# Kernel optimization log

Hardware: AMD Instinct MI355X
Metric: run time of the kernel (lower is better)

Reference implementation:

```python
import jax, jax.numpy as jnp
import numpy as np

T, B, H, K = 512, 64, 512, 16  # seq_len, batch, hidden_size, num_tags


def setup_inputs() -> dict:
    key = jax.random.key(0)
    ks = jax.random.split(key, 8)
    hidden = jax.random.normal(ks[0], (T, B, H), dtype=jnp.float32)
    W1 = jax.random.normal(ks[1], (H, H), dtype=jnp.float32) / np.float32(np.sqrt(H))
    b1 = jnp.zeros((H,), jnp.float32)
    W2 = jax.random.normal(ks[2], (H, K), dtype=jnp.float32) / np.float32(np.sqrt(H))
    b2 = jnp.zeros((K,), jnp.float32)
    transition = jax.random.normal(ks[3], (K, K), dtype=jnp.float32)
    lens = jax.random.randint(ks[4], (B,), T // 2, T + 1)  # valid lengths in [T/2, T]
    tags = jax.random.randint(ks[5], (T, B), 0, K)
    return dict(hidden=hidden, W1=W1, b1=b1, W2=W2, b2=b2,
                transition=transition, lens=lens, tags=tags)


def reference(hidden, W1, b1, W2, b2, transition, lens, tags):
    # Emission MLP (dropout is identity in eval): Linear -> ReLU -> Linear
    h = jax.nn.relu(hidden @ W1 + b1)          # [T, B, H]
    em = h @ W2 + b2                           # [T, B, K]

    # ---- forward (partition) score: linear-chain logsumexp DP ----
    def step(alpha, e_t):
        # alpha: [B, K] over prev tags; transition[curr, prev]
        a = jax.nn.logsumexp(alpha[:, None, :] + transition[None, :, :], axis=-1) + e_t
        return a, a

    alpha0 = em[0]
    _, alphas = jax.lax.scan(step, alpha0, em[1:])
    alphas = jnp.concatenate([alpha0[None], alphas], axis=0)            # [T, B, K]
    last = jnp.take_along_axis(alphas, (lens - 1)[None, :, None], axis=0)[0]  # [B, K]
    fwd_score = jax.nn.logsumexp(last, axis=-1)                          # [B]

    # ---- gold path score ----
    em_path = jnp.take_along_axis(em, tags[:, :, None], axis=-1)[..., 0]  # [T, B]
    trans_path = transition[tags[1:], tags[:-1]]                          # [T-1, B]
    steps = em_path.at[1:].add(trans_path)
    cum = jnp.cumsum(steps, axis=0)                                       # [T, B]
    gold = jnp.take_along_axis(cum, (lens - 1)[None, :], axis=0)[0]       # [B]

    return (fwd_score - gold).sum()
```

## Files before the change

### kernel.cpp

```cpp
#include <hip/hip_runtime.h>
#include <hip/hip_bf16.h>

#define TT 512
#define BB 64
#define HH 512
#define KK 16

#define NCH 16
#define CST (TT / NCH)

typedef __attribute__((ext_vector_type(8))) short bf16x8;
typedef __attribute__((ext_vector_type(4))) short bf16x4;
typedef __attribute__((ext_vector_type(4))) float f32x4;

#define MFMA_K16(A, B, C) __builtin_amdgcn_mfma_f32_16x16x16bf16_1k(A, B, C, 0, 0, 0)

__device__ __forceinline__ unsigned short f2bf(float f) {
    union { __hip_bfloat16 h; unsigned short u; } cvt;
    cvt.h = __float2bfloat16(f);
    return cvt.u;
}

__device__ __forceinline__ short rne_bf(float x) {
    unsigned u = __float_as_uint(x);
    u += 0x7fffu + ((u >> 16) & 1u);
    return (short)(u >> 16);
}

__device__ __forceinline__ float bf2f(short s) {
    return __uint_as_float(((unsigned)(unsigned short)s) << 16);
}

__global__ void prep_kernel(const float* __restrict__ W1, const float* __restrict__ W2,
                            unsigned short* __restrict__ W1t, unsigned short* __restrict__ W2t,
                            float* __restrict__ out) {
    const int bi = blockIdx.x, tx = threadIdx.x;
    if (bi < 64) {
        __shared__ float Ls[64][65];
        const int ti = bi & 7, tj = bi >> 3;
        const int r0 = ti * 64, c0 = tj * 64;
        const int r = tx >> 4, c4 = (tx & 15) * 4;
#pragma unroll
        for (int i = 0; i < 4; ++i) {
            float4 v = *(const float4*)(W1 + (size_t)(r0 + r + 16 * i) * HH + c0 + c4);
            Ls[c4 + 0][r + 16 * i] = v.x;
            Ls[c4 + 1][r + 16 * i] = v.y;
            Ls[c4 + 2][r + 16 * i] = v.z;
            Ls[c4 + 3][r + 16 * i] = v.w;
        }
        __syncthreads();
        const int rn = tx >> 4, k4 = (tx & 15) * 4;
#pragma unroll
        for (int i = 0; i < 4; ++i) {
            const int n = rn + 16 * i;
            ushort4 o;
            o.x = f2bf(Ls[n][k4 + 0]);
            o.y = f2bf(Ls[n][k4 + 1]);
            o.z = f2bf(Ls[n][k4 + 2]);
            o.w = f2bf(Ls[n][k4 + 3]);
            *(ushort4*)(W1t + (size_t)(c0 + n) * HH + r0 + k4) = o;
        }
    } else {
        if (tx == 0) out[0] = 0.0f;
        for (int idx = tx; idx < 16 * HH; idx += 256) {
            const int n = idx >> 9, k = idx & 511;
            W2t[idx] = f2bf(W2[k * KK + n]);
        }
    }
}

__global__ __launch_bounds__(256, 2)
void em_kernel(const float* __restrict__ hidden, const unsigned short* __restrict__ W1t,
               const float* __restrict__ b1, const unsigned short* __restrict__ W2t,
               const float* __restrict__ b2, float* __restrict__ em) {
    __shared__ __align__(16) unsigned char stage[74752];
    unsigned short* const As = (unsigned short*)stage;
    unsigned short* const Bs = (unsigned short*)(stage + 9216);

    const int tx = threadIdx.x;
    const int w = tx >> 6, lane = tx & 63;
    const int q = lane >> 4, nl = lane & 15;
    const int wm = w >> 1, wn = w & 1;
    const int row0 = blockIdx.x * 64;

    f32x4 acc[2][16];
#pragma unroll
    for (int mt = 0; mt < 2; ++mt)
#pragma unroll
        for (int nt = 0; nt < 16; ++nt) acc[mt][nt] = (f32x4){0.f, 0.f, 0.f, 0.f};

    for (int kt = 0; kt < 8; ++kt) {
        const int k0 = kt * 64;
        __syncthreads();
        {
            const int r = tx >> 2, c16 = (tx & 3) * 16;
            const float* src = hidden + (size_t)(row0 + r) * HH + k0 + c16;
            float4 v0 = *(const float4*)(src);
            float4 v1 = *(const float4*)(src + 4);
            float4 v2 = *(const float4*)(src + 8);
            float4 v3 = *(const float4*)(src + 12);
            bf16x8 o0, o1;
            o0[0] = (short)f2bf(v0.x); o0[1] = (short)f2bf(v0.y);
            o0[2] = (short)f2bf(v0.z); o0[3] = (short)f2bf(v0.w);
            o0[4] = (short)f2bf(v1.x); o0[5] = (short)f2bf(v1.y);
            o0[6] = (short)f2bf(v1.z); o0[7] = (short)f2bf(v1.w);
            o1[0] = (short)f2bf(v2.x); o1[1] = (short)f2bf(v2.y);
            o1[2] = (short)f2bf(v2.z); o1[3] = (short)f2bf(v2.w);
            o1[4] = (short)f2bf(v3.x); o1[5] = (short)f2bf(v3.y);
            o1[6] = (short)f2bf(v3.z); o1[7] = (short)f2bf(v3.w);
            *(bf16x8*)(As + r * 72 + c16) = o0;
            *(bf16x8*)(As + r * 72 + c16 + 8) = o1;
        }
#pragma unroll
        for (int it = 0; it < 16; ++it) {
            const int c = it * 256 + tx;
            const int n = c >> 3, slot = c & 7;
            const int kc = slot ^ (n & 7);
            __builtin_amdgcn_global_load_lds(
                (const __attribute__((address_space(1))) void*)(W1t + (size_t)n * HH + k0 + kc * 8),
                (__attribute__((address_space(3))) void*)(Bs + c * 8),
                16, 0, 0);
        }
        __syncthreads();
        bf16x8 af[2][2];
#pragma unroll
        for (int mt = 0; mt < 2; ++mt)
#pragma unroll
            for (int kk = 0; kk < 2; ++kk)
                af[mt][kk] = *(const bf16x8*)(As + (32 * wm + 16 * mt + nl) * 72 + kk * 32 + q * 8);
#pragma unroll
        for (int nt = 0; nt < 16; ++nt) {
            const int n = 256 * wn + 16 * nt + nl;
#pragma unroll
            for (int kk = 0; kk < 2; ++kk) {
                const int slot = (4 * kk + q) ^ (n & 7);
                bf16x8 bf = *(const bf16x8*)(Bs + n * 64 + slot * 8);
                acc[0][nt] = __builtin_amdgcn_mfma_f32_16x16x32_bf16(af[0][kk], bf, acc[0][nt], 0, 0, 0);
                acc[1][nt] = __builtin_amdgcn_mfma_f32_16x16x32_bf16(af[1][kk], bf, acc[1][nt], 0, 0, 0);
            }
        }
    }

    __syncthreads();
    unsigned short* const Hb  = (unsigned short*)stage;
    unsigned short* const W2s = (unsigned short*)(stage + 33792);
#pragma unroll
    for (int i = tx; i < 1024; i += 256) {
        const int n = i >> 6, kc = i & 63;
        *(bf16x8*)(W2s + n * 520 + kc * 8) = *(const bf16x8*)(W2t + n * HH + kc * 8);
    }

    f32x4 acc2 = (f32x4){0.f, 0.f, 0.f, 0.f};
#pragma unroll
    for (int c = 0; c < 2; ++c) {
        if (wn == c) {
#pragma unroll
            for (int nt = 0; nt < 16; ++nt) {
                const float bv = b1[c * 256 + 16 * nt + nl];
#pragma unroll
                for (int mt = 0; mt < 2; ++mt) {
#pragma unroll
                    for (int r = 0; r < 4; ++r) {
                        float v = acc[mt][nt][r] + bv;
                        v = v > 0.f ? v : 0.f;
                        const int row = 32 * wm + 16 * mt + q * 4 + r;
                        Hb[row * 264 + nt * 16 + nl] = f2bf(v);
                    }
                }
            }
        }
        __syncthreads();
#pragma unroll
        for (int ks = 0; ks < 8; ++ks) {
            bf16x8 a2 = *(const bf16x8*)(Hb + (16 * w + nl) * 264 + ks * 32 + q * 8);
            bf16x8 b2f = *(const bf16x8*)(W2s + nl * 520 + c * 256 + ks * 32 + q * 8);
            acc2 = __builtin_amdgcn_mfma_f32_16x16x32_bf16(a2, b2f, acc2, 0, 0, 0);
        }
        __syncthreads();
    }
#pragma unroll
    for (int r = 0; r < 4; ++r) {
        const int row = row0 + 16 * w + q * 4 + r;
        em[(size_t)row * KK + nl] = acc2[r] + b2[nl];
    }
}

__global__ void scan_gold_kernel(const float* __restrict__ em, const float* __restrict__ trans,
                                 const int* __restrict__ lens, const int* __restrict__ tags,
                                 float* __restrict__ Pfull, float* __restrict__ Cfull,
                                 float* __restrict__ Ppart, float* __restrict__ Cpart,
                                 float* __restrict__ out) {
    __shared__ float trs[256];
    __shared__ float red[4];
    const int tx = threadIdx.x;

    if (blockIdx.x >= 256) {
        trs[tx] = __logf(bf2f(rne_bf(__expf(trans[tx]))));
        __syncthreads();
        const int idx = (blockIdx.x - 256) * 256 + tx;
        const int t = idx >> 6, b = idx & 63;
        const int L = lens[b];
        float v = 0.0f;
        if (t < L) {
            const int tg = tags[t * BB + b];
            v = em[((size_t)t * BB + b) * KK + tg];
            if (t > 0) v += trs[tg * 16 + tags[(t - 1) * BB + b]];
        }
#pragma unroll
        for (int dd = 1; dd < 64; dd <<= 1) v += __shfl_xor(v, dd, 64);
        if ((tx & 63) == 0) red[tx >> 6] = v;
        __syncthreads();
        if (tx == 0) atomicAdd(out, -(red[0] + red[1] + red[2] + red[3]));
        return;
    }

    const int id = blockIdx.x * 4 + (tx >> 6);
    const int lane = tx & 63, q = lane >> 4, col = lane & 15;
    const int b = id >> 4, c = id & 15;

    float mf[4];
    {
        float4 tv = *(const float4*)(trans + col * 16 + 4 * q);
        mf[0] = bf2f(rne_bf(__expf(tv.x)));
        mf[1] = bf2f(rne_bf(__expf(tv.y)));
        mf[2] = bf2f(rne_bf(__expf(tv.z)));
        mf[3] = bf2f(rne_bf(__expf(tv.w)));
    }
    const int Lm1 = lens[b] - 1;
    const int tb0 = CST * c;

    float ebuf[8];
#pragma unroll
    for (int i = 0; i < 8; ++i)
        ebuf[i] = em[(size_t)((tb0 + i) * BB + b) * KK + col];

    bf16x4 gb;
#pragma unroll
    for (int i = 0; i < 4; ++i)
        gb[i] = (4 * q + i == col) ? rne_bf(1.0f) : (short)0;

    const f32x4 zc = (f32x4){0.f, 0.f, 0.f, 0.f};
    f32x4 d = (f32x4){0.f, 0.f, 0.f, 0.f};
    float K = 1.0f, rk = 1.0f, lk = 0.0f, Cacc = 0.0f;

    for (int sb = 0; sb < CST; sb += 8) {
        const bool refill = (sb < CST - 8);
#pragma unroll
        for (int s8 = 0; s8 < 8; ++s8) {
            const int t = tb0 + sb + s8;
            const float eraw = ebuf[s8];
            if (refill)
                ebuf[s8] = em[(size_t)((t + 8) * BB + b) * KK + col];
            float ev = __expf(eraw);
            if ((s8 & 3) == 0 && (sb + s8) >= 4) {
                ev *= rk;
                Cacc += lk;
            }
            bf16x4 af;
            af[0] = rne_bf(ev * mf[0]); af[1] = rne_bf(ev * mf[1]);
            af[2] = rne_bf(ev * mf[2]); af[3] = rne_bf(ev * mf[3]);
            if (s8 == 0) {
                if (sb == 0 && c == 0) {
#pragma unroll
                    for (int i = 0; i < 4; ++i)
                        af[i] = (4 * q + i == col) ? rne_bf(ev) : (short)0;
                }
            }
            d = MFMA_K16(af, gb, zc);
            if ((s8 & 3) == 1) {
                K = __shfl(d[0], 0, 64);
                const float Km = fmaxf(K, 1e-30f);
                rk = 1.0f / Km;
                lk = __logf(Km);
            }
            if (t == Lm1) {
#pragma unroll
                for (int r = 0; r < 4; ++r)
                    Ppart[b * 256 + (4 * q + r) * 16 + col] = d[r];
                if (lane == 0) Cpart[b] = Cacc;
            }
            gb[0] = rne_bf(d[0]); gb[1] = rne_bf(d[1]);
            gb[2] = rne_bf(d[2]); gb[3] = rne_bf(d[3]);
        }
    }
#pragma unroll
    for (int r = 0; r < 4; ++r)
        Pfull[(size_t)(b * NCH + c) * 256 + (4 * q + r) * 16 + col] = d[r];
    if (lane == 0) Cfull[b * NCH + c] = Cacc;
}

__global__ void combine_kernel(const int* __restrict__ lens,
                               const float* __restrict__ Pfull, const float* __restrict__ Cfull,
                               const float* __restrict__ Ppart, const float* __restrict__ Cpart,
                               float* __restrict__ out) {
    const int lane = threadIdx.x;
    const int grp = lane >> 4, j = lane & 15;
    const int b = blockIdx.x * 4 + grp;
    const int base = grp << 4;
    const int cstar = (lens[b] - 1) / CST;

    float g = 1.0f, acc = 0.0f;
    for (int c = 0; c < NCH; ++c) {
        const bool act = (c <= cstar);
        const float* P = (c < cstar) ? (Pfull + (size_t)(b * NCH + c) * 256)
                                     : (Ppart + b * 256);
        float gn = 0.0f;
#pragma unroll
        for (int k = 0; k < 16; ++k) {
            const float gk = __shfl(g, base + k, 64);
            gn += P[j * 16 + k] * gk;
        }
        if (act) {
            float m = gn;
#pragma unroll
            for (int dd = 1; dd < 16; dd <<= 1) m = fmaxf(m, __shfl_xor(m, dd, 64));
            g = gn / m;
            acc += __logf(m) + ((c < cstar) ? Cfull[b * NCH + c] : Cpart[b]);
        }
    }
    float ssum = g;
#pragma unroll
    for (int dd = 1; dd < 16; dd <<= 1) ssum += __shfl_xor(ssum, dd, 64);
    const float fwd = acc + __logf(ssum);
    if (j == 0) atomicAdd(out, fwd);
}

extern "C" void kernel_launch(void* const* d_in, const int* in_sizes, int n_in,
                              void* d_out, int out_size, void* d_ws, size_t ws_size,
                              hipStream_t stream) {
    const float* hidden = (const float*)d_in[0];
    const float* W1     = (const float*)d_in[1];
    const float* b1     = (const float*)d_in[2];
    const float* W2     = (const float*)d_in[3];
    const float* b2     = (const float*)d_in[4];
    const float* trans  = (const float*)d_in[5];
    const int*   lens   = (const int*)d_in[6];
    const int*   tags   = (const int*)d_in[7];
    float* out = (float*)d_out;

    char* ws = (char*)d_ws;
    float* em = (float*)ws;
    unsigned short* W1t = (unsigned short*)(ws + 2097152);
    unsigned short* W2t = (unsigned short*)(ws + 2621440);
    float* Pfull = (float*)(ws + 2637824);
    float* Cfull = (float*)(ws + 3686400);
    float* Ppart = (float*)(ws + 3690496);
    float* Cpart = (float*)(ws + 3756032);

    prep_kernel<<<65, 256, 0, stream>>>(W1, W2, W1t, W2t, out);
    em_kernel<<<512, 256, 0, stream>>>(hidden, W1t, b1, W2t, b2, em);
    scan_gold_kernel<<<384, 256, 0, stream>>>(em, trans, lens, tags,
                                              Pfull, Cfull, Ppart, Cpart, out);
    combine_kernel<<<16, 64, 0, stream>>>(lens, Pfull, Cfull, Ppart, Cpart, out);
}
```

Before: 146.0 us.

## Fuse gold-path scoring into emission kernel and simplify second GEMM staging

Moves the gold-path score computation out of the scan kernel and into the emission GEMM epilogue, where each block already holds the emissions for one timestep, so em no longer has to be re-read for the gold score. The second GEMM now writes the full 512-wide ReLU activation to LDS once and reads W2 directly from global memory. This removes the W2 staging copy and the two-pass loop with its extra barriers. The trade-off is more epilogue work and an atomic per em block, plus uncached global reads of W2 inside the MFMA loop.

```diff
diff --git a/kernel.cpp b/kernel.cpp
--- a/kernel.cpp
+++ b/kernel.cpp
@@ -72,8 +72,12 @@
 __global__ __launch_bounds__(256, 2)
 void em_kernel(const float* __restrict__ hidden, const unsigned short* __restrict__ W1t,
                const float* __restrict__ b1, const unsigned short* __restrict__ W2t,
-               const float* __restrict__ b2, float* __restrict__ em) {
+               const float* __restrict__ b2, const float* __restrict__ trans,
+               const int* __restrict__ lens, const int* __restrict__ tags,
+               float* __restrict__ em, float* __restrict__ out) {
     __shared__ __align__(16) unsigned char stage[74752];
+    __shared__ float trs[256];
+    __shared__ float red[4];
     unsigned short* const As = (unsigned short*)stage;
     unsigned short* const Bs = (unsigned short*)(stage + 9216);
 
@@ -81,7 +85,10 @@
     const int w = tx >> 6, lane = tx & 63;
     const int q = lane >> 4, nl = lane & 15;
     const int wm = w >> 1, wn = w & 1;
-    const int row0 = blockIdx.x * 64;
+    const int t = blockIdx.x;
+    const int row0 = t * 64;
+
+    trs[tx] = __logf(bf2f(rne_bf(__expf(trans[tx]))));
 
     f32x4 acc[2][16];
 #pragma unroll
@@ -142,78 +149,56 @@
     }
 
     __syncthreads();
-    unsigned short* const Hb  = (unsigned short*)stage;
-    unsigned short* const W2s = (unsigned short*)(stage + 33792);
-#pragma unroll
-    for (int i = tx; i < 1024; i += 256) {
-        const int n = i >> 6, kc = i & 63;
-        *(bf16x8*)(W2s + n * 520 + kc * 8) = *(const bf16x8*)(W2t + n * HH + kc * 8);
-    }
-
+    unsigned short* const Hb = (unsigned short*)stage;
+#pragma unroll
+    for (int nt = 0; nt < 16; ++nt) {
+        const float bv = b1[256 * wn + 16 * nt + nl];
+#pragma unroll
+        for (int mt = 0; mt < 2; ++mt) {
+#pragma unroll
+            for (int r = 0; r < 4; ++r) {
+                float v = acc[mt][nt][r] + bv;
+                v = v > 0.f ? v : 0.f;
+                Hb[(32 * wm + 16 * mt + q * 4 + r) * 520 + 256 * wn + 16 * nt + nl] = f2bf(v);
+            }
+        }
+    }
+    __syncthreads();
     f32x4 acc2 = (f32x4){0.f, 0.f, 0.f, 0.f};
 #pragma unroll
-    for (int c = 0; c < 2; ++c) {
-        if (wn == c) {
-#pragma unroll
-            for (int nt = 0; nt < 16; ++nt) {
-                const float bv = b1[c * 256 + 16 * nt + nl];
-#pragma unroll
-                for (int mt = 0; mt < 2; ++mt) {
-#pragma unroll
-                    for (int r = 0; r < 4; ++r) {
-                        float v = acc[mt][nt][r] + bv;
-                        v = v > 0.f ? v : 0.f;
-                        const int row = 32 * wm + 16 * mt + q * 4 + r;
-                        Hb[row * 264 + nt * 16 + nl] = f2bf(v);
-                    }
-                }
-            }
-        }
-        __syncthreads();
-#pragma unroll
-        for (int ks = 0; ks < 8; ++ks) {
-            bf16x8 a2 = *(const bf16x8*)(Hb + (16 * w + nl) * 264 + ks * 32 + q * 8);
-            bf16x8 b2f = *(const bf16x8*)(W2s + nl * 520 + c * 256 + ks * 32 + q * 8);
-            acc2 = __builtin_amdgcn_mfma_f32_16x16x32_bf16(a2, b2f, acc2, 0, 0, 0);
-        }
-        __syncthreads();
-    }
+    for (int ks = 0; ks < 16; ++ks) {
+        bf16x8 a2  = *(const bf16x8*)(Hb + (16 * w + nl) * 520 + ks * 32 + q * 8);
+        bf16x8 b2f = *(const bf16x8*)(W2t + (size_t)nl * HH + ks * 32 + q * 8);
+        acc2 = __builtin_amdgcn_mfma_f32_16x16x32_bf16(a2, b2f, acc2, 0, 0, 0);
+    }
+
+    float gv = 0.0f;
 #pragma unroll
     for (int r = 0; r < 4; ++r) {
-        const int row = row0 + 16 * w + q * 4 + r;
-        em[(size_t)row * KK + nl] = acc2[r] + b2[nl];
-    }
-}
-
-__global__ void scan_gold_kernel(const float* __restrict__ em, const float* __restrict__ trans,
-                                 const int* __restrict__ lens, const int* __restrict__ tags,
-                                 float* __restrict__ Pfull, float* __restrict__ Cfull,
-                                 float* __restrict__ Ppart, float* __restrict__ Cpart,
-                                 float* __restrict__ out) {
-    __shared__ float trs[256];
-    __shared__ float red[4];
+        const int b = 16 * w + q * 4 + r;
+        const float ev = acc2[r] + b2[nl];
+        em[(size_t)(row0 + b) * KK + nl] = ev;
+        if (t < lens[b]) {
+            const int tg = tags[(size_t)t * BB + b];
+            if (nl == tg) {
+                float v = ev;
+                if (t > 0) v += trs[tg * 16 + tags[(size_t)(t - 1) * BB + b]];
+                gv += v;
+            }
+        }
+    }
+#pragma unroll
+    for (int dd = 1; dd < 64; dd <<= 1) gv += __shfl_xor(gv, dd, 64);
+    if (lane == 0) red[w] = gv;
+    __syncthreads();
+    if (tx == 0) atomicAdd(out, -(red[0] + red[1] + red[2] + red[3]));
+}
+
+__global__ void scan_kernel(const float* __restrict__ em, const float* __restrict__ trans,
+                            const int* __restrict__ lens,
+                            float* __restrict__ Pfull, float* __restrict__ Cfull,
+                            float* __restrict__ Ppart, float* __restrict__ Cpart) {
     const int tx = threadIdx.x;
-
-    if (blockIdx.x >= 256) {
-        trs[tx] = __logf(bf2f(rne_bf(__expf(trans[tx]))));
-        __syncthreads();
-        const int idx = (blockIdx.x - 256) * 256 + tx;
-        const int t = idx >> 6, b = idx & 63;
-        const int L = lens[b];
-        float v = 0.0f;
-        if (t < L) {
-            const int tg = tags[t * BB + b];
-            v = em[((size_t)t * BB + b) * KK + tg];
-            if (t > 0) v += trs[tg * 16 + tags[(t - 1) * BB + b]];
-        }
-#pragma unroll
-        for (int dd = 1; dd < 64; dd <<= 1) v += __shfl_xor(v, dd, 64);
-        if ((tx & 63) == 0) red[tx >> 6] = v;
-        __syncthreads();
-        if (tx == 0) atomicAdd(out, -(red[0] + red[1] + red[2] + red[3]));
-        return;
-    }
-
     const int id = blockIdx.x * 4 + (tx >> 6);
     const int lane = tx & 63, q = lane >> 4, col = lane & 15;
     const int b = id >> 4, c = id & 15;
@@ -348,8 +333,9 @@
     float* Cpart = (float*)(ws + 3756032);
 
     prep_kernel<<<65, 256, 0, stream>>>(W1, W2, W1t, W2t, out);
-    em_kernel<<<512, 256, 0, stream>>>(hidden, W1t, b1, W2t, b2, em);
-    scan_gold_kernel<<<384, 256, 0, stream>>>(em, trans, lens, tags,
-                                              Pfull, Cfull, Ppart, Cpart, out);
+    em_kernel<<<512, 256, 0, stream>>>(hidden, W1t, b1, W2t, b2, trans,
+                                       lens, tags, em, out);
+    scan_kernel<<<256, 256, 0, stream>>>(em, trans, lens,
+                                         Pfull, Cfull, Ppart, Cpart);
     combine_kernel<<<16, 64, 0, stream>>>(lens, Pfull, Cfull, Ppart, Cpart, out);
 }
```

Result: slower. 150.5 us (+3.1%).
